# Kernel optimization log

Hardware: AMD Instinct MI355X
Metric: run time of the kernel (lower is better)

## Reference

```python
import jax, jax.numpy as jnp
import numpy as np

S = 30.0   # scale
M = 0.3    # additive angular margin (arcface)
EPS = 1e-07


def setup_inputs() -> dict:
    key = jax.random.key(0)
    k1, k2, k3 = jax.random.split(key, 3)
    N, D, C = 8192, 256, 10000
    x = jax.random.normal(k1, (N, D), dtype=jnp.float32)
    W = jax.random.normal(k2, (C, D), dtype=jnp.float32) * 0.05  # linear weight [C, D]
    target = jax.random.randint(k3, (N,), 0, C)
    return {"x": x, "W": W, "target": target}


def reference(x, W, target):
    # L2-normalize inputs along features. NOTE: the torch code's loop that
    # 'normalizes' weight_fc params is a no-op (rebinds a local), so W is
    # intentionally NOT normalized here, matching the original math.
    xn = x / jnp.linalg.norm(x, axis=1, keepdims=True)
    logits = xn @ W.T                                   # [N, C]
    n = logits.shape[0]
    tgt = logits[jnp.arange(n), target]                 # [N] target-class cosine-like score
    # arcface margin: s * cos(acos(clamp(t)) + m)
    numerator = S * jnp.cos(jnp.arccos(jnp.clip(tgt, -1.0 + EPS, 1.0 - EPS)) + M)
    # exclude-target sum: sum_j exp(s*logits) minus the target column (no [N,C-1] concat)
    exp_s = jnp.exp(S * logits)                         # [N, C]
    sum_excl = jnp.sum(exp_s, axis=1) - jnp.exp(S * tgt)
    denominator = jnp.exp(numerator) + sum_excl
    L = numerator - jnp.log(denominator)
    return -jnp.mean(L)
```

## Files before the change

kernel.cpp:

```cpp
#include <hip/hip_runtime.h>
#include <hip/hip_bf16.h>
#include <stdint.h>

#define S_SCALE 30.0f
#define S_L2E_SC 0.33813165020835f
#define N_ROWS 8192
#define D_DIM 256
#define C_CLS 10000
#define NCB 8

typedef __attribute__((ext_vector_type(4))) float f32x4;

static __device__ __forceinline__ void gl16(const void* g, void* l) {
  __builtin_amdgcn_global_load_lds(
      (const __attribute__((address_space(1))) void*)g,
      (__attribute__((address_space(3))) void*)l, 16, 0, 0);
}

static __device__ __forceinline__ long u2l(uint2 v) {
  union { uint2 u; long l; } x; x.u = v; return x.l;
}

static __device__ __forceinline__ float row_sum16(float v) {
  union { float f; int i; } u, w;
  u.f = v;
  w.i = __builtin_amdgcn_update_dpp(0, u.i, 0xB1, 0xF, 0xF, true);  u.f += w.f;
  w.i = __builtin_amdgcn_update_dpp(0, u.i, 0x4E, 0xF, 0xF, true);  u.f += w.f;
  w.i = __builtin_amdgcn_update_dpp(0, u.i, 0x141, 0xF, 0xF, true); u.f += w.f;
  w.i = __builtin_amdgcn_update_dpp(0, u.i, 0x140, 0xF, 0xF, true); u.f += w.f;
  return u.f;
}

__global__ __launch_bounds__(256) void k_prep(const float* __restrict__ x,
                                              const float* __restrict__ W,
                                              const int* __restrict__ target,
                                              unsigned char* __restrict__ xnb8,
                                              unsigned char* __restrict__ WbF8,
                                              float* __restrict__ tgt) {
  if (blockIdx.x < 1280) {
    int gidx = blockIdx.x * 256 + threadIdx.x;
    int lane = gidx & 63;
    int kc = (gidx >> 6) & 7;
    int c16 = gidx >> 9;
    int col = c16 * 16 + (lane & 15);
    int k0 = kc * 32 + (lane >> 4) * 8;
    int r0 = 0, r1 = 0;
    if (col < C_CLS) {
      const float4 a = *(const float4*)(W + (size_t)col * D_DIM + k0);
      const float4 b = *(const float4*)(W + (size_t)col * D_DIM + k0 + 4);
      r0 = __builtin_amdgcn_cvt_pk_fp8_f32(a.x * 16.f, a.y * 16.f, 0, false);
      r0 = __builtin_amdgcn_cvt_pk_fp8_f32(a.z * 16.f, a.w * 16.f, r0, true);
      r1 = __builtin_amdgcn_cvt_pk_fp8_f32(b.x * 16.f, b.y * 16.f, 0, false);
      r1 = __builtin_amdgcn_cvt_pk_fp8_f32(b.z * 16.f, b.w * 16.f, r1, true);
    }
    *(int2*)(WbF8 + (size_t)gidx * 8) = (int2){r0, r1};
  } else {
    int row = (blockIdx.x - 1280) * 4 + (threadIdx.x >> 6);
    int l = threadIdx.x & 63;
    const float4 v = *(const float4*)(x + (size_t)row * D_DIM + l * 4);
    float ss = v.x * v.x + v.y * v.y + v.z * v.z + v.w * v.w;
#pragma unroll
    for (int m = 1; m < 64; m <<= 1) ss += __shfl_xor(ss, m, 64);
    float rn = 1.0f / sqrtf(ss);
    float s8 = rn * 8.f;
    int r0 = __builtin_amdgcn_cvt_pk_fp8_f32(v.x * s8, v.y * s8, 0, false);
    r0 = __builtin_amdgcn_cvt_pk_fp8_f32(v.z * s8, v.w * s8, r0, true);
    int panel = row >> 7, r16 = (row >> 4) & 7, lr = row & 15;
    size_t dst = (size_t)panel * 32768 + (size_t)(r16 * 8 + (l >> 3)) * 512 +
                 (size_t)(((l >> 1) & 3) * 16 + lr) * 8 + (l & 1) * 4;
    *(int*)(xnb8 + dst) = r0;
    int tc = target[row];
    const float4 b = *(const float4*)(W + (size_t)tc * D_DIM + l * 4);
    float s = v.x * b.x + v.y * b.y + v.z * b.z + v.w * b.w;
#pragma unroll
    for (int m = 1; m < 64; m <<= 1) s += __shfl_xor(s, m, 64);
    if (l == 0) tgt[row] = s * rn;
  }
}

__global__ __launch_bounds__(512, 4) void k_gemm(const unsigned char* __restrict__ xnb8,
                                                 const unsigned char* __restrict__ WbF8,
                                                 float* __restrict__ partials) {
  __shared__ __align__(16) char lds[34816];
  const int b = blockIdx.x;
  const int cg = b & 7;
  const int br = b >> 3;
  const int bc0 = cg * 5;
  const int t = threadIdx.x;
  const int w = t >> 6, l = t & 63;
  const int wr = w >> 2, wc = w & 3;
  const int lr = l & 15, lk = l >> 4;
  float* rsumAll = (float*)(lds + 32768);

  if (t < 512) rsumAll[t] = 0.f;

  {
    const char* Ag = (const char*)xnb8 + (size_t)br * 32768;
#pragma unroll
    for (int i = 0; i < 4; ++i)
      gl16(Ag + i * 8192 + w * 1024 + l * 16, lds + i * 8192 + w * 1024);
    asm volatile("s_waitcnt vmcnt(0)" ::: "memory");
    __builtin_amdgcn_sched_barrier(0);
    __builtin_amdgcn_s_barrier();
  }

  f32x4 acc[4][4];
#pragma unroll
  for (int m = 0; m < 4; m++)
#pragma unroll
    for (int n = 0; n < 4; n++) acc[m][n] = (f32x4){0.f, 0.f, 0.f, 0.f};

  const char* AwL = lds + (size_t)(wr * 4 * 8) * 512 + (size_t)l * 8;
  const unsigned char* Bw = WbF8 + (size_t)(bc0 * 16 + wc * 4) * 4096 + (size_t)l * 8;
  float* rw = rsumAll + w * 64;

  uint2 b0[4], b1[4];
#pragma unroll
  for (int fn = 0; fn < 4; ++fn) b0[fn] = *(const uint2*)(Bw + fn * 4096);

  for (int tt = 0; tt < 5; ++tt) {
    auto step = [&](int kc, uint2(&cur)[4], uint2(&nxt)[4]) {
      if (kc < 7) {
#pragma unroll
        for (int fn = 0; fn < 4; ++fn)
          nxt[fn] = *(const uint2*)(Bw + fn * 4096 + (kc + 1) * 512);
      } else if (tt < 4) {
#pragma unroll
        for (int fn = 0; fn < 4; ++fn)
          nxt[fn] = *(const uint2*)(Bw + 65536 + fn * 4096);
      }
      __builtin_amdgcn_s_setprio(1);
#pragma unroll
      for (int fm = 0; fm < 4; ++fm) {
        long a = u2l(*(const uint2*)(AwL + (fm * 8 + kc) * 512));
#pragma unroll
        for (int fn = 0; fn < 4; ++fn)
          acc[fm][fn] = __builtin_amdgcn_mfma_f32_16x16x32_fp8_fp8(
              a, u2l(cur[fn]), acc[fm][fn], 0, 0, 0);
      }
      __builtin_amdgcn_s_setprio(0);
    };
    step(0, b0, b1); step(1, b1, b0); step(2, b0, b1); step(3, b1, b0);
    step(4, b0, b1); step(5, b1, b0); step(6, b0, b1); step(7, b1, b0);

#pragma unroll
    for (int m = 0; m < 4; ++m) {
      float rs0 = 0.f, rs1 = 0.f, rs2 = 0.f, rs3 = 0.f;
#pragma unroll
      for (int n = 0; n < 4; ++n) {
        rs0 += __builtin_amdgcn_exp2f(acc[m][n][0] * S_L2E_SC);
        rs1 += __builtin_amdgcn_exp2f(acc[m][n][1] * S_L2E_SC);
        rs2 += __builtin_amdgcn_exp2f(acc[m][n][2] * S_L2E_SC);
        rs3 += __builtin_amdgcn_exp2f(acc[m][n][3] * S_L2E_SC);
        acc[m][n] = (f32x4){0.f, 0.f, 0.f, 0.f};
      }
      rs0 = row_sum16(rs0); rs1 = row_sum16(rs1);
      rs2 = row_sum16(rs2); rs3 = row_sum16(rs3);
      if (lr == 0) {
        int row = m * 16 + lk * 4;
        rw[row + 0] += rs0; rw[row + 1] += rs1;
        rw[row + 2] += rs2; rw[row + 3] += rs3;
      }
    }
    Bw += 65536;
  }

  __syncthreads();
  if (t < 128) {
    int wr2 = t >> 6, r = t & 63;
    float sv = rsumAll[(wr2 * 4 + 0) * 64 + r] + rsumAll[(wr2 * 4 + 1) * 64 + r] +
               rsumAll[(wr2 * 4 + 2) * 64 + r] + rsumAll[(wr2 * 4 + 3) * 64 + r];
    partials[(size_t)cg * N_ROWS + (size_t)br * 128 + t] = sv;
  }
}

__global__ __launch_bounds__(256) void k_loss1(const float* __restrict__ partials,
                                               const float* __restrict__ tgt,
                                               float* __restrict__ bsum) {
  __shared__ float wsum[4];
  int i = blockIdx.x * 256 + threadIdx.x;
  const float* p = partials + i;
  float s = -240.0f;
#pragma unroll
  for (int j = 0; j < NCB; ++j) s += p[(size_t)j * N_ROWS];
  float tl = tgt[i];
  float tcv = fminf(fmaxf(tl, -1.0f + 1e-7f), 1.0f - 1e-7f);
  const float cm = 0.95533648912560601964f;
  const float sm = 0.29552020666133957510f;
  float num = S_SCALE * (tcv * cm - sqrtf(fmaxf(1.0f - tcv * tcv, 0.f)) * sm);
  float sum_excl = s - __expf(S_SCALE * tl);
  float denom = __expf(num) + sum_excl;
  float L = num - __logf(denom);
#pragma unroll
  for (int m = 1; m < 64; m <<= 1) L += __shfl_xor(L, m, 64);
  int l = threadIdx.x & 63, w = threadIdx.x >> 6;
  if (l == 0) wsum[w] = L;
  __syncthreads();
  if (threadIdx.x == 0) bsum[blockIdx.x] = wsum[0] + wsum[1] + wsum[2] + wsum[3];
}

__global__ void k_loss2(const float* __restrict__ bsum, float* __restrict__ out) {
  float s = 0.f;
  for (int i = 0; i < 32; ++i) s += bsum[i];
  out[0] = -s / (float)N_ROWS;
}

extern "C" void kernel_launch(void* const* d_in, const int* in_sizes, int n_in,
                              void* d_out, int out_size, void* d_ws, size_t ws_size,
                              hipStream_t stream) {
  const float* x = (const float*)d_in[0];
  const float* W = (const float*)d_in[1];
  const int* target = (const int*)d_in[2];
  float* out = (float*)d_out;
  char* ws = (char*)d_ws;

  unsigned char* xnb8 = (unsigned char*)(ws);
  unsigned char* WbF8 = (unsigned char*)(ws + 2097152);
  float* tgt = (float*)(ws + 4718592);
  float* partials = (float*)(ws + 4751360);
  float* bsum = (float*)(ws + 5013504);

  k_prep<<<3328, 256, 0, stream>>>(x, W, target, xnb8, WbF8, tgt);
  k_gemm<<<512, 512, 0, stream>>>(xnb8, WbF8, partials);
  k_loss1<<<32, 256, 0, stream>>>(partials, tgt, bsum);
  k_loss2<<<1, 1, 0, stream>>>(bsum, out);
}
```

Measured before the change: 50.10 us.

## Interleave FP8 weight tiles for 16-byte loads and stagger tile order per wave

The prep kernel now writes W's FP8 fragments so that two adjacent 16-column groups sit next to each other per lane. This lets the GEMM load B operands as two 16-byte loads instead of four 8-byte loads per k-step. Each wave also starts its pass over the five column tiles at a different offset (w % 5), spreading global/L2 accesses across waves. Row-sum accumulation order changes but results stay equivalent up to float rounding.

Measured after the change: 50.25 us. About the same (+0.3%).

```diff
diff --git a/kernel.cpp b/kernel.cpp
--- a/kernel.cpp
+++ b/kernel.cpp
@@ -53,7 +53,9 @@
       r1 = __builtin_amdgcn_cvt_pk_fp8_f32(b.x * 16.f, b.y * 16.f, 0, false);
       r1 = __builtin_amdgcn_cvt_pk_fp8_f32(b.z * 16.f, b.w * 16.f, r1, true);
     }
-    *(int2*)(WbF8 + (size_t)gidx * 8) = (int2){r0, r1};
+    size_t dst = (size_t)(c16 >> 1) * 8192 + (size_t)kc * 1024 +
+                 (size_t)lane * 16 + (size_t)(c16 & 1) * 8;
+    *(int2*)(WbF8 + dst) = (int2){r0, r1};
   } else {
     int row = (blockIdx.x - 1280) * 4 + (threadIdx.x >> 6);
     int l = threadIdx.x & 63;
@@ -111,32 +113,43 @@
     for (int n = 0; n < 4; n++) acc[m][n] = (f32x4){0.f, 0.f, 0.f, 0.f};
 
   const char* AwL = lds + (size_t)(wr * 4 * 8) * 512 + (size_t)l * 8;
-  const unsigned char* Bw = WbF8 + (size_t)(bc0 * 16 + wc * 4) * 4096 + (size_t)l * 8;
+  const unsigned char* Bwv = WbF8 + (size_t)(bc0 * 8 + wc * 2) * 8192 + (size_t)l * 16;
   float* rw = rsumAll + w * 64;
 
-  uint2 b0[4], b1[4];
-#pragma unroll
-  for (int fn = 0; fn < 4; ++fn) b0[fn] = *(const uint2*)(Bw + fn * 4096);
-
-  for (int tt = 0; tt < 5; ++tt) {
-    auto step = [&](int kc, uint2(&cur)[4], uint2(&nxt)[4]) {
+  const int tt0 = w % 5;
+  uint4 b0[2], b1[2];
+  {
+    const unsigned char* Bt = Bwv + (size_t)tt0 * 65536;
+    b0[0] = *(const uint4*)(Bt);
+    b0[1] = *(const uint4*)(Bt + 8192);
+  }
+
+  for (int s = 0; s < 5; ++s) {
+    int tt = tt0 + s; if (tt >= 5) tt -= 5;
+    int ttn = tt + 1; if (ttn >= 5) ttn -= 5;
+    const unsigned char* Bt = Bwv + (size_t)tt * 65536;
+    const unsigned char* Btn = Bwv + (size_t)ttn * 65536;
+
+    auto step = [&](int kc, uint4(&cur)[2], uint4(&nxt)[2]) {
       if (kc < 7) {
-#pragma unroll
-        for (int fn = 0; fn < 4; ++fn)
-          nxt[fn] = *(const uint2*)(Bw + fn * 4096 + (kc + 1) * 512);
-      } else if (tt < 4) {
-#pragma unroll
-        for (int fn = 0; fn < 4; ++fn)
-          nxt[fn] = *(const uint2*)(Bw + 65536 + fn * 4096);
+        nxt[0] = *(const uint4*)(Bt + (kc + 1) * 1024);
+        nxt[1] = *(const uint4*)(Bt + 8192 + (kc + 1) * 1024);
+      } else if (s < 4) {
+        nxt[0] = *(const uint4*)(Btn);
+        nxt[1] = *(const uint4*)(Btn + 8192);
       }
       __builtin_amdgcn_s_setprio(1);
 #pragma unroll
       for (int fm = 0; fm < 4; ++fm) {
         long a = u2l(*(const uint2*)(AwL + (fm * 8 + kc) * 512));
-#pragma unroll
-        for (int fn = 0; fn < 4; ++fn)
-          acc[fm][fn] = __builtin_amdgcn_mfma_f32_16x16x32_fp8_fp8(
-              a, u2l(cur[fn]), acc[fm][fn], 0, 0, 0);
+        acc[fm][0] = __builtin_amdgcn_mfma_f32_16x16x32_fp8_fp8(
+            a, u2l((uint2){cur[0].x, cur[0].y}), acc[fm][0], 0, 0, 0);
+        acc[fm][1] = __builtin_amdgcn_mfma_f32_16x16x32_fp8_fp8(
+            a, u2l((uint2){cur[0].z, cur[0].w}), acc[fm][1], 0, 0, 0);
+        acc[fm][2] = __builtin_amdgcn_mfma_f32_16x16x32_fp8_fp8(
+            a, u2l((uint2){cur[1].x, cur[1].y}), acc[fm][2], 0, 0, 0);
+        acc[fm][3] = __builtin_amdgcn_mfma_f32_16x16x32_fp8_fp8(
+            a, u2l((uint2){cur[1].z, cur[1].w}), acc[fm][3], 0, 0, 0);
       }
       __builtin_amdgcn_s_setprio(0);
     };
@@ -162,7 +175,6 @@
         rw[row + 2] += rs2; rw[row + 3] += rs3;
       }
     }
-    Bw += 65536;
   }
 
   __syncthreads();
```
